# Optimization experiments

Measured on AMD Instinct MI355X. Metric: run time of the kernel, lower is better.

The kernel has to match this reference:

```python
import jax, jax.numpy as jnp
import numpy as np

B, C_IN, C_OUT, N, K = 4, 128, 128, 4096, 32
BN_EPS = 1e-5


def setup_inputs() -> dict:
    key = jax.random.key(0)
    ks = jax.random.split(key, 12)
    x = jax.random.normal(ks[0], (B, C_IN, N), jnp.float32)
    feature = jax.random.normal(ks[1], (B, C_OUT, N, K), jnp.float32)
    graph_index = jax.random.randint(ks[2], (B, N, K), 0, N)
    s_in = 1.0 / np.sqrt(C_IN)
    s_out = 1.0 / np.sqrt(C_OUT)
    # theta_x: Conv2d(C_IN -> C_IN, 1x1), shared for theta and phi branches
    Wt = jax.random.uniform(ks[3], (C_IN, C_IN), jnp.float32, -s_in, s_in)
    bt = jax.random.uniform(ks[4], (C_IN,), jnp.float32, -s_in, s_in)
    # g: Conv2d(C_OUT -> C_OUT, 1x1)
    Wg = jax.random.uniform(ks[5], (C_OUT, C_OUT), jnp.float32, -s_out, s_out)
    bg = jax.random.uniform(ks[6], (C_OUT,), jnp.float32, -s_out, s_out)
    # W: Conv1d(C_OUT -> C_OUT, 1) followed by BatchNorm1d(C_OUT)
    Ww = jax.random.uniform(ks[7], (C_OUT, C_OUT), jnp.float32, -s_out, s_out)
    bw = jax.random.uniform(ks[8], (C_OUT,), jnp.float32, -s_out, s_out)
    gamma = jnp.ones((C_OUT,), jnp.float32)
    beta = jnp.zeros((C_OUT,), jnp.float32)
    return {"graph_index": graph_index, "x": x, "feature": feature,
            "Wt": Wt, "bt": bt, "Wg": Wg, "bg": bg,
            "Ww": Ww, "bw": bw, "gamma": gamma, "beta": beta}


def reference(graph_index, x, feature, Wt, bt, Wg, bg, Ww, bw, gamma, beta):
    b, c, n = x.shape
    # torch does x.contiguous().view(B, N, C) -> a reshape, not a transpose
    xr = x.reshape(b, n, c)                                   # [B,N,C]
    # index_points: per-batch gather of k neighbors
    batch_idx = jnp.arange(b)[:, None, None]
    nb = xr[batch_idx, graph_index]                           # [B,N,K,C]
    # theta_x 1x1 conv applied to centre and to neighbors (shared weights)
    theta = jnp.einsum('bnc,dc->bnd', xr, Wt) + bt            # [B,N,C]
    phi = jnp.einsum('bnkc,dc->bnkd', nb, Wt) + bt            # [B,N,K,C]
    # local attention logits over k neighbors, softmax over k
    logits = jnp.einsum('bnd,bnkd->bnk', theta, phi)          # [B,N,K]
    coef = jax.nn.softmax(logits, axis=-1)                    # [B,N,K]
    # g 1x1 conv on neighbor value features
    gx = jnp.einsum('bcnk,dc->bnkd', feature, Wg) + bg        # [B,N,K,Cout]
    # weighted aggregation over neighbors
    out = jnp.einsum('bnk,bnkd->bnd', coef, gx)               # [B,N,Cout]
    # W: 1x1 Conv1d then BatchNorm1d (training-mode batch stats)
    y = jnp.einsum('bnd,ed->ben', out, Ww) + bw[None, :, None]  # [B,Cout,N]
    mean = jnp.mean(y, axis=(0, 2), keepdims=True)
    var = jnp.var(y, axis=(0, 2), keepdims=True)
    z = (y - mean) * jax.lax.rsqrt(var + BN_EPS)
    z = z * gamma[None, :, None] + beta[None, :, None]
    return z
```

## Files before the change

kernel.cpp:

```cpp
#include <hip/hip_runtime.h>
#include <hip/hip_bf16.h>

#define BB 4
#define CC 128
#define NN 4096
#define KK 32
#define THETA_OFF 0
#define THETA_SZ  (BB*NN*CC)
#define AGG_OFF   (THETA_OFF + THETA_SZ)
#define AGG_SZ    (BB*NN*CC)
#define M_OFF     (AGG_OFF + AGG_SZ)
#define M_SZ      (CC*CC)
#define B2_OFF    (M_OFF + M_SZ)
#define COEF_OFF  (B2_OFF + 128)
#define COEF_SZ   (BB*NN*KK)
#define PART_OFF  (COEF_OFF + COEF_SZ)
#define PART_SZ   (512*256)
#define PART2_OFF (PART_OFF + PART_SZ)
#define PART2_SZ  (64*256)
#define STAT_OFF  (PART2_OFF + PART2_SZ)

__device__ __forceinline__ float dot4(float4 a, float4 b) {
    return a.x*b.x + a.y*b.y + a.z*b.z + a.w*b.w;
}

__device__ __forceinline__ void async_copy16(const float* g, float* l) {
    __builtin_amdgcn_global_load_lds(
        (const __attribute__((address_space(1))) void*)g,
        (__attribute__((address_space(3))) void*)l, 16, 0, 0);
}

__global__ __launch_bounds__(256) void kWT(const float* __restrict__ x,
                                           const float* __restrict__ Wt,
                                           const float* __restrict__ bt,
                                           const float* __restrict__ Ww,
                                           const float* __restrict__ Wg,
                                           const float* __restrict__ bg,
                                           const float* __restrict__ bw,
                                           float* __restrict__ theta,
                                           float* __restrict__ M,
                                           float* __restrict__ b2) {
    __shared__ float xr[32][132];
    __shared__ float wt[128][36];
    int t = threadIdx.x;
    if (blockIdx.x >= 512) {
        int bid2 = blockIdx.x - 512;
        if (bid2 < 64) {
            int e = bid2 * 2 + (t >> 7);
            int c = t & 127;
            float acc = 0.f;
#pragma unroll 8
            for (int d = 0; d < 128; ++d)
                acc += Ww[e*128 + d] * Wg[d*128 + c];
            M[e*128 + c] = acc;
        } else if (t < 128) {
            float acc = bw[t];
            for (int d = 0; d < 128; ++d)
                acc += Ww[t*128 + d] * bg[d];
            b2[t] = acc;
        }
        return;
    }
    long base = (long)blockIdx.x * (32 * 128);
#pragma unroll
    for (int r = 0; r < 4; ++r) {
        int f = (t + 256*r) * 4;
        int dn = f >> 7, c = f & 127;
        *(float4*)&xr[dn][c] = *(const float4*)(x + base + f);
    }
    float acc[4][4] = {};
    int e0 = t & 31, dn0 = (t >> 5) * 4;
    for (int cb = 0; cb < 4; ++cb) {
        __syncthreads();
#pragma unroll
        for (int r = 0; r < 4; ++r) {
            int f = (t + 256*r) * 4;
            int d = f >> 5, cc = f & 31;
            *(float4*)&wt[d][cc] = *(const float4*)(Wt + d*128 + cb*32 + cc);
        }
        __syncthreads();
#pragma unroll
        for (int q = 0; q < 8; ++q) {
            float4 a4[4], m4[4];
#pragma unroll
            for (int j = 0; j < 4; ++j) a4[j] = *(const float4*)&xr[dn0+j][cb*32 + q*4];
#pragma unroll
            for (int i = 0; i < 4; ++i) m4[i] = *(const float4*)&wt[e0 + 32*i][q*4];
#pragma unroll
            for (int i = 0; i < 4; ++i)
#pragma unroll
                for (int j = 0; j < 4; ++j)
                    acc[i][j] += dot4(a4[j], m4[i]);
        }
    }
    __syncthreads();
#pragma unroll
    for (int i = 0; i < 4; ++i) {
        float b = bt[e0 + 32*i];
#pragma unroll
        for (int j = 0; j < 4; ++j)
            xr[dn0 + j][e0 + 32*i] = acc[i][j] + b;
    }
    __syncthreads();
#pragma unroll
    for (int r = 0; r < 4; ++r) {
        int f = (t + 256*r) * 4;
        int dn = f >> 7, c = f & 127;
        *(float4*)(theta + base + f) = *(const float4*)&xr[dn][c];
    }
}

__global__ __launch_bounds__(256) void kA(const int* __restrict__ gi,
                                          const float* __restrict__ theta,
                                          float* __restrict__ coefG) {
    __shared__ float tc[16][132];
    __shared__ float logits[16][33];
    int t = threadIdx.x;
    long trow0 = (long)blockIdx.x * 16;
    int b = blockIdx.x >> 8;
    int k = t >> 3, l8 = t & 7;
#pragma unroll
    for (int r = 0; r < 2; ++r) {
        int f = (t + 256*r) * 4;
        int dn = f >> 7, c = f & 127;
        *(float4*)&tc[dn][c] = *(const float4*)(theta + trow0*128 + f);
    }
    int idxs[16];
#pragma unroll
    for (int dn = 0; dn < 16; ++dn)
        idxs[dn] = gi[(trow0 + dn) * KK + k];
    __syncthreads();
    const float* tbat = theta + (long)b * NN * CC;
#pragma unroll 2
    for (int dn = 0; dn < 16; ++dn) {
        const float* row = tbat + (long)idxs[dn] * CC;
        float p = 0.f;
#pragma unroll
        for (int j = 0; j < 4; ++j) {
            int c = j*32 + l8*4;
            float4 g = *(const float4*)(row + c);
            float4 tcv = *(const float4*)&tc[dn][c];
            p += dot4(g, tcv);
        }
        p += __shfl_xor(p, 1);
        p += __shfl_xor(p, 2);
        p += __shfl_xor(p, 4);
        if (l8 == 0) logits[dn][k] = p;
    }
    __syncthreads();
    if (t < 128) {
        int row = t >> 3;
        float l[4];
#pragma unroll
        for (int j = 0; j < 4; ++j) l[j] = logits[row][l8 + 8*j];
        float m = fmaxf(fmaxf(l[0], l[1]), fmaxf(l[2], l[3]));
        m = fmaxf(m, __shfl_xor(m, 1));
        m = fmaxf(m, __shfl_xor(m, 2));
        m = fmaxf(m, __shfl_xor(m, 4));
        float e[4]; float s = 0.f;
#pragma unroll
        for (int j = 0; j < 4; ++j) { e[j] = __expf(l[j] - m); s += e[j]; }
        s += __shfl_xor(s, 1);
        s += __shfl_xor(s, 2);
        s += __shfl_xor(s, 4);
        float inv = 1.0f / s;
#pragma unroll
        for (int j = 0; j < 4; ++j)
            coefG[(trow0 + row) * KK + l8 + 8*j] = e[j] * inv;
    }
}

__global__ __launch_bounds__(256) void kB(const float* __restrict__ coefG,
                                          const float* __restrict__ feat,
                                          float* __restrict__ aggG) {
    __shared__ float stage[2][4][32][32];
    __shared__ float aggL[32][36];
    int t = threadIdx.x;
    int cc4 = blockIdx.x & 3;
    int tile = blockIdx.x >> 2;
    int b = tile >> 7;
    int n0 = (tile & 127) * 32;
    int dn = t >> 3, l8 = t & 7;
    int w = t >> 6, lane = t & 63;
    int r = lane >> 3, s = lane & 7;
    int rot = ((s - r) & 7) * 4;

    float4 cf = *(const float4*)(coefG + ((size_t)tile * 32 + dn) * KK + l8 * 4);

    const size_t S = (size_t)NN * KK;
    const float* fbase = feat + ((size_t)b * CC + cc4 * 32) * S + (size_t)n0 * KK;

    {
        const float* fc = fbase + (size_t)w * S;
#pragma unroll
        for (int i = 0; i < 4; ++i)
            async_copy16(fc + (i*8 + r)*KK + rot, &stage[0][w][i*8][0]);
    }
    __syncthreads();
    int buf = 0;
    for (int ch = 0; ch < 8; ++ch) {
        if (ch < 7) {
            const float* fc = fbase + (size_t)((ch+1)*4 + w) * S;
#pragma unroll
            for (int i = 0; i < 4; ++i)
                async_copy16(fc + (i*8 + r)*KK + rot, &stage[buf^1][w][i*8][0]);
        }
#pragma unroll
        for (int cl = 0; cl < 4; ++cl) {
            float4 f = *(const float4*)&stage[buf][cl][dn][((l8 + dn) & 7) * 4];
            float v = dot4(f, cf);
            v += __shfl_xor(v, 1);
            v += __shfl_xor(v, 2);
            v += __shfl_xor(v, 4);
            if (l8 == 0) aggL[dn][ch*4 + cl] = v;
        }
        __syncthreads();
        buf ^= 1;
    }
    int row = t >> 3, col4 = l8 * 4;
    *(float4*)(aggG + ((size_t)b * NN + n0 + row) * CC + cc4 * 32 + col4) =
        *(const float4*)&aggL[row][col4];
}

__global__ __launch_bounds__(256) void kC(const float* __restrict__ aggG,
                                          const float* __restrict__ Mmat,
                                          const float* __restrict__ b2v,
                                          float* __restrict__ y,
                                          float* __restrict__ partial) {
    __shared__ float agg[32][132];
    __shared__ float mc[128][36];
    __shared__ float pw[4][128];
    __shared__ float qw[4][128];
    int t = threadIdx.x;
    int b = blockIdx.x >> 7;
    int n0 = (blockIdx.x & 127) * 32;
    long base = (long)blockIdx.x * (32 * 128);
#pragma unroll
    for (int r = 0; r < 4; ++r) {
        int f = (t + 256*r) * 4;
        int dn = f >> 7, c = f & 127;
        *(float4*)&agg[dn][c] = *(const float4*)(aggG + base + f);
    }
    float acc[4][4] = {};
    int e0 = t & 31, dn0 = (t >> 5) * 4;
    for (int cb = 0; cb < 4; ++cb) {
        __syncthreads();
#pragma unroll
        for (int r = 0; r < 4; ++r) {
            int f = (t + 256*r) * 4;
            int e = f >> 5, cc = f & 31;
            *(float4*)&mc[e][cc] = *(const float4*)(Mmat + e*128 + cb*32 + cc);
        }
        __syncthreads();
#pragma unroll
        for (int q = 0; q < 8; ++q) {
            float4 a4[4], m4[4];
#pragma unroll
            for (int j = 0; j < 4; ++j) a4[j] = *(const float4*)&agg[dn0+j][cb*32 + q*4];
#pragma unroll
            for (int i = 0; i < 4; ++i) m4[i] = *(const float4*)&mc[e0 + 32*i][q*4];
#pragma unroll
            for (int i = 0; i < 4; ++i)
#pragma unroll
                for (int j = 0; j < 4; ++j)
                    acc[i][j] += dot4(a4[j], m4[i]);
        }
        __syncthreads();
    }
    int w = t >> 6;
#pragma unroll
    for (int i = 0; i < 4; ++i) {
        int e = e0 + 32*i;
        float bb = b2v[e];
        float4 yv;
        yv.x = acc[i][0] + bb;
        yv.y = acc[i][1] + bb;
        yv.z = acc[i][2] + bb;
        yv.w = acc[i][3] + bb;
        *(float4*)(y + ((long)(b*CC + e)) * NN + n0 + dn0) = yv;
        float s = yv.x + yv.y + yv.z + yv.w;
        float qq = yv.x*yv.x + yv.y*yv.y + yv.z*yv.z + yv.w*yv.w;
        s  += __shfl_xor(s, 32);
        qq += __shfl_xor(qq, 32);
        if (!(t & 32)) { pw[w][e] = s; qw[w][e] = qq; }
    }
    __syncthreads();
    if (t < 128) {
        partial[(long)blockIdx.x * 256 + t]       = pw[0][t] + pw[1][t] + pw[2][t] + pw[3][t];
        partial[(long)blockIdx.x * 256 + 128 + t] = qw[0][t] + qw[1][t] + qw[2][t] + qw[3][t];
    }
}

__global__ __launch_bounds__(256) void kR1(const float* __restrict__ partial,
                                           float* __restrict__ partial2) {
    int t = threadIdx.x;
    long b0 = (long)blockIdx.x * 8;
    float acc = 0.f;
#pragma unroll
    for (int j = 0; j < 8; ++j)
        acc += partial[(b0 + j) * 256 + t];
    partial2[(long)blockIdx.x * 256 + t] = acc;
}

__global__ __launch_bounds__(256) void kR2(const float* __restrict__ partial2,
                                           const float* __restrict__ gamma,
                                           const float* __restrict__ beta,
                                           float* __restrict__ stats) {
    __shared__ float buf[256];
    int t = threadIdx.x;
    float acc = 0.f;
#pragma unroll
    for (int j = 0; j < 64; ++j)
        acc += partial2[j * 256 + t];
    buf[t] = acc;
    __syncthreads();
    if (t < 128) {
        float S = buf[t], Q = buf[t + 128];
        const float invN = 1.0f / (BB * NN);
        float mean = S * invN;
        float var  = Q * invN - mean * mean;
        float sc = rsqrtf(var + 1e-5f) * gamma[t];
        stats[t]       = sc;
        stats[128 + t] = beta[t] - mean * sc;
    }
}

__global__ void kZ(float* __restrict__ y, const float* __restrict__ stats) {
    int idx = blockIdx.x * 256 + threadIdx.x;
#pragma unroll
    for (int r = 0; r < 2; ++r) {
        int i = idx + r * 262144;
        int e = (i >> 10) & 127;
        float sc = stats[e], sh = stats[128 + e];
        float4 v = ((float4*)y)[i];
        v.x = v.x * sc + sh;
        v.y = v.y * sc + sh;
        v.z = v.z * sc + sh;
        v.w = v.w * sc + sh;
        ((float4*)y)[i] = v;
    }
}

extern "C" void kernel_launch(void* const* d_in, const int* in_sizes, int n_in,
                              void* d_out, int out_size, void* d_ws, size_t ws_size,
                              hipStream_t stream) {
    const int*   gi    = (const int*)d_in[0];
    const float* x     = (const float*)d_in[1];
    const float* feat  = (const float*)d_in[2];
    const float* Wt    = (const float*)d_in[3];
    const float* bt    = (const float*)d_in[4];
    const float* Wg    = (const float*)d_in[5];
    const float* bg    = (const float*)d_in[6];
    const float* Ww    = (const float*)d_in[7];
    const float* bw    = (const float*)d_in[8];
    const float* gamma = (const float*)d_in[9];
    const float* beta  = (const float*)d_in[10];

    float* y  = (float*)d_out;
    float* ws = (float*)d_ws;
    float* theta    = ws + THETA_OFF;
    float* aggG     = ws + AGG_OFF;
    float* Mmat     = ws + M_OFF;
    float* b2       = ws + B2_OFF;
    float* coefG    = ws + COEF_OFF;
    float* partial  = ws + PART_OFF;
    float* partial2 = ws + PART2_OFF;
    float* stats    = ws + STAT_OFF;

    kWT<<<577, 256, 0, stream>>>(x, Wt, bt, Ww, Wg, bg, bw, theta, Mmat, b2);
    kA<<<1024, 256, 0, stream>>>(gi, theta, coefG);
    kB<<<2048, 256, 0, stream>>>(coefG, feat, aggG);
    kC<<<512, 256, 0, stream>>>(aggG, Mmat, b2, y, partial);
    kR1<<<64, 256, 0, stream>>>(partial, partial2);
    kR2<<<1, 256, 0, stream>>>(partial2, gamma, beta, stats);
    kZ<<<1024, 256, 0, stream>>>(y, stats);
}
```

Before: 114.0 us.

## Triple-buffer feature loads in kB with explicit vmcnt waits; swizzle kA block order

```diff
diff --git a/kernel.cpp b/kernel.cpp
--- a/kernel.cpp
+++ b/kernel.cpp
@@ -30,6 +30,10 @@
         (__attribute__((address_space(3))) void*)l, 16, 0, 0);
 }
 
+#define SYNCB() do { asm volatile("" ::: "memory"); \
+                     __builtin_amdgcn_s_barrier(); \
+                     asm volatile("" ::: "memory"); } while (0)
+
 __global__ __launch_bounds__(256) void kWT(const float* __restrict__ x,
                                            const float* __restrict__ Wt,
                                            const float* __restrict__ bt,
@@ -116,8 +120,9 @@
     __shared__ float tc[16][132];
     __shared__ float logits[16][33];
     int t = threadIdx.x;
-    long trow0 = (long)blockIdx.x * 16;
-    int b = blockIdx.x >> 8;
+    int bid = (blockIdx.x & 7) * 128 + (blockIdx.x >> 3);
+    long trow0 = (long)bid * 16;
+    int b = bid >> 8;
     int k = t >> 3, l8 = t & 7;
 #pragma unroll
     for (int r = 0; r < 2; ++r) {
@@ -173,7 +178,7 @@
 __global__ __launch_bounds__(256) void kB(const float* __restrict__ coefG,
                                           const float* __restrict__ feat,
                                           float* __restrict__ aggG) {
-    __shared__ float stage[2][4][32][32];
+    __shared__ float stage[3][4][32][32];
     __shared__ float aggL[32][36];
     int t = threadIdx.x;
     int cc4 = blockIdx.x & 3;
@@ -182,41 +187,50 @@
     int n0 = (tile & 127) * 32;
     int dn = t >> 3, l8 = t & 7;
     int w = t >> 6, lane = t & 63;
-    int r = lane >> 3, s = lane & 7;
-    int rot = ((s - r) & 7) * 4;
 
     float4 cf = *(const float4*)(coefG + ((size_t)tile * 32 + dn) * KK + l8 * 4);
+    asm volatile("" :: "v"(cf.x), "v"(cf.y), "v"(cf.z), "v"(cf.w));
 
     const size_t S = (size_t)NN * KK;
-    const float* fbase = feat + ((size_t)b * CC + cc4 * 32) * S + (size_t)n0 * KK;
-
-    {
-        const float* fc = fbase + (size_t)w * S;
+    const float* fbase = feat + ((size_t)b * CC + cc4 * 32) * S + (size_t)n0 * KK + lane * 4;
+
+#pragma unroll
+    for (int ch = 0; ch < 3; ++ch) {
+        const float* fc = fbase + (size_t)(ch * 4 + w) * S;
+        float* ld = &stage[ch][w][0][0];
 #pragma unroll
         for (int i = 0; i < 4; ++i)
-            async_copy16(fc + (i*8 + r)*KK + rot, &stage[0][w][i*8][0]);
-    }
-    __syncthreads();
-    int buf = 0;
+            async_copy16(fc + i * 256, ld + i * 256);
+    }
+
+    int slot = 0;
+#pragma unroll
     for (int ch = 0; ch < 8; ++ch) {
-        if (ch < 7) {
-            const float* fc = fbase + (size_t)((ch+1)*4 + w) * S;
-#pragma unroll
-            for (int i = 0; i < 4; ++i)
-                async_copy16(fc + (i*8 + r)*KK + rot, &stage[buf^1][w][i*8][0]);
-        }
+        int rem = 7 - ch;
+        if (rem >= 2)      asm volatile("s_waitcnt vmcnt(8)" ::: "memory");
+        else if (rem == 1) asm volatile("s_waitcnt vmcnt(4)" ::: "memory");
+        else               asm volatile("s_waitcnt vmcnt(0)" ::: "memory");
+        SYNCB();
 #pragma unroll
         for (int cl = 0; cl < 4; ++cl) {
-            float4 f = *(const float4*)&stage[buf][cl][dn][((l8 + dn) & 7) * 4];
+            float4 f = *(const float4*)&stage[slot][cl][dn][l8 * 4];
             float v = dot4(f, cf);
             v += __shfl_xor(v, 1);
             v += __shfl_xor(v, 2);
             v += __shfl_xor(v, 4);
-            if (l8 == 0) aggL[dn][ch*4 + cl] = v;
-        }
-        __syncthreads();
-        buf ^= 1;
-    }
+            if (l8 == 0) aggL[dn][ch * 4 + cl] = v;
+        }
+        SYNCB();
+        if (ch + 3 < 8) {
+            const float* fc = fbase + (size_t)((ch + 3) * 4 + w) * S;
+            float* ld = &stage[slot][w][0][0];
+#pragma unroll
+            for (int i = 0; i < 4; ++i)
+                async_copy16(fc + i * 256, ld + i * 256);
+        }
+        slot = (slot == 2) ? 0 : slot + 1;
+    }
+    __syncthreads();
     int row = t >> 3, col4 = l8 * 4;
     *(float4*)(aggG + ((size_t)b * NN + n0 + row) * CC + cc4 * 32 + col4) =
         *(const float4*)&aggL[row][col4];
```

Measured after the change: 107.2 us. 5.9% less time.
